# Performance work log

Hardware: AMD Instinct MI355X
Metric: run time of the kernel (lower is better)

## Reference

```python
import jax, jax.numpy as jnp
import numpy as np

N_NODES = 100000
N_EDGES = 1600000
IN_CH = 128
HID = 128
OUT_CH = 40


def setup_inputs() -> dict:
    key = jax.random.key(0)
    ks = jax.random.split(key, 8)
    x = jax.random.normal(ks[0], (N_NODES, IN_CH), dtype=jnp.float32)
    edge_index = jax.random.randint(ks[1], (2, N_EDGES), 0, N_NODES, dtype=jnp.int64)
    s1 = 1.0 / np.sqrt(IN_CH)
    s2 = 1.0 / np.sqrt(HID)
    # SAGEConv layer 1: lin_l (applied to aggregated neighbors, has bias), lin_r (applied to root, no bias)
    Wl1 = jax.random.uniform(ks[2], (IN_CH, HID), jnp.float32, -s1, s1)
    b1 = jnp.zeros((HID,), jnp.float32)
    Wr1 = jax.random.uniform(ks[3], (IN_CH, HID), jnp.float32, -s1, s1)
    # SAGEConv layer 2
    Wl2 = jax.random.uniform(ks[4], (HID, OUT_CH), jnp.float32, -s2, s2)
    b2 = jnp.zeros((OUT_CH,), jnp.float32)
    Wr2 = jax.random.uniform(ks[5], (HID, OUT_CH), jnp.float32, -s2, s2)
    return {"x": x, "edge_index": edge_index, "Wl1": Wl1, "b1": b1, "Wr1": Wr1,
            "Wl2": Wl2, "b2": b2, "Wr2": Wr2}


def _sage_conv(x, src, dst, Wl, b, Wr):
    # mean-aggregate source-node features onto target nodes (PyG SAGEConv, aggr='mean')
    msg_sum = jax.ops.segment_sum(x[src], dst, num_segments=N_NODES)  # [N, F]
    deg = jax.ops.segment_sum(jnp.ones((src.shape[0],), x.dtype), dst, num_segments=N_NODES)
    aggr = msg_sum / jnp.maximum(deg, 1.0)[:, None]
    return aggr @ Wl + b + x @ Wr


def reference(x, edge_index, Wl1, b1, Wr1, Wl2, b2, Wr2):
    src, dst = edge_index[0], edge_index[1]
    h = _sage_conv(x, src, dst, Wl1, b1, Wr1)
    h = jax.nn.relu(h)  # dropout is identity in eval mode
    h = _sage_conv(h, src, dst, Wl2, b2, Wr2)
    return jax.nn.log_softmax(h, axis=-1)
```

## Files before the change

### kernel.cpp

```cpp
#include <hip/hip_runtime.h>
#include <math.h>

#define NN 100000
#define NE 1600000
#define NBUK ((NN + 255) / 256)
#define CAP 5120
#define NBLK_A 500
#define EPB (NE / NBLK_A)
#define GPB (EPB / 4)
#define MT ((NN + 127) / 128)
#define MPAD ((size_t)MT * 128)
#define PACK_B 192
#define CVT_B0 (NBLK_A + PACK_B)
#define FRONT_GRID 2048

typedef __attribute__((ext_vector_type(8))) short short8;
typedef __attribute__((ext_vector_type(4))) float f32x4;
typedef __attribute__((ext_vector_type(4))) int i32x4;
typedef unsigned short ushort_t;
typedef unsigned int uint_t;

__device__ inline ushort_t f2bf(float f) {
    uint_t u = __builtin_bit_cast(uint_t, f);
    u += 0x7FFFu + ((u >> 16) & 1u);
    return (ushort_t)(u >> 16);
}
__device__ inline float bits2f(uint_t u) { return __builtin_bit_cast(float, u); }
__device__ inline float lo16(uint_t u) { return bits2f(u << 16); }
__device__ inline float hi16(uint_t u) { return bits2f(u & 0xFFFF0000u); }

__device__ inline void gload_lds16(const void* g, void* l) {
    __builtin_amdgcn_global_load_lds(
        (const __attribute__((address_space(1))) unsigned int*)g,
        (__attribute__((address_space(3))) unsigned int*)l, 16, 0, 0);
}

__global__ __launch_bounds__(256) void front(const float* __restrict__ x,
                                             ushort_t* __restrict__ xb,
                                             const float* __restrict__ Wl1,
                                             const float* __restrict__ Wr1,
                                             const float* __restrict__ Wl2,
                                             const float* __restrict__ Wr2,
                                             ushort_t* __restrict__ W1T,
                                             ushort_t* __restrict__ W2T,
                                             const int* __restrict__ ei,
                                             int* __restrict__ bhist) {
    __shared__ int h[NBUK];
    int bid = blockIdx.x, tid = threadIdx.x;
    if (bid < NBLK_A) {
        for (int i = tid; i < NBUK; i += 256) h[i] = 0;
        __syncthreads();
        const i32x4* dsts = (const i32x4*)(ei + NE + bid * EPB);
        for (int g = tid; g < GPB; g += 256) {
            i32x4 d = __builtin_nontemporal_load(dsts + g);
#pragma unroll
            for (int j = 0; j < 4; ++j) atomicAdd(&h[d[j] >> 8], 1);
        }
        __syncthreads();
        for (int i = tid; i < NBUK; i += 256)
            if (h[i]) atomicAdd(&bhist[i], h[i]);
    } else if (bid < CVT_B0) {
        int gid = (bid - NBLK_A) * 256 + tid;
        if (gid < 256 * 128) {
            int n = gid >> 7, k = gid & 127;
            float v = (n < 128) ? Wl1[k * 128 + n] : Wr1[k * 128 + (n - 128)];
            W1T[gid] = f2bf(v);
        } else {
            int g = gid - 256 * 128;
            if (g < 128 * 128) {
                int n = g >> 7, k = g & 127;
                float v = 0.0f;
                if (n < 40)      v = Wl2[k * 40 + n];
                else if (n < 80) v = Wr2[k * 40 + (n - 40)];
                W2T[g] = f2bf(v);
            }
        }
    } else {
        const int total = NN * 128 / 8;
        const int nb = FRONT_GRID - CVT_B0;
        const f32x4* src = (const f32x4*)x;
        for (int g = (bid - CVT_B0) * 256 + tid; g < total; g += nb * 256) {
            f32x4 v0 = __builtin_nontemporal_load(src + (size_t)g * 2);
            f32x4 v1 = __builtin_nontemporal_load(src + (size_t)g * 2 + 1);
            i32x4 o;
            o[0] = ((uint_t)f2bf(v0[1]) << 16) | (uint_t)f2bf(v0[0]);
            o[1] = ((uint_t)f2bf(v0[3]) << 16) | (uint_t)f2bf(v0[2]);
            o[2] = ((uint_t)f2bf(v1[1]) << 16) | (uint_t)f2bf(v1[0]);
            o[3] = ((uint_t)f2bf(v1[3]) << 16) | (uint_t)f2bf(v1[2]);
            *(i32x4*)(xb + (size_t)g * 8) = o;
        }
    }
}

__global__ __launch_bounds__(512) void scan_buckets(const int* __restrict__ bhist,
                                                    int* __restrict__ boff,
                                                    int* __restrict__ gcur,
                                                    int* __restrict__ offsets) {
    __shared__ int part[512];
    int t = threadIdx.x;
    int v = (t < NBUK) ? bhist[t] : 0;
    part[t] = v;
    __syncthreads();
    for (int d = 1; d < 512; d <<= 1) {
        int tmp = (t >= d) ? part[t - d] : 0;
        __syncthreads();
        part[t] += tmp;
        __syncthreads();
    }
    if (t <= NBUK) {
        int excl = (t == 0) ? 0 : part[t - 1];
        boff[t] = excl;
        if (t < NBUK) gcur[t] = excl;
    }
    if (t == 0) offsets[NN] = NE;
}

__global__ __launch_bounds__(256) void bin_pass(const int* __restrict__ ei,
                                                int* __restrict__ gcur,
                                                int* __restrict__ pairs) {
    __shared__ int h[NBUK];
    __shared__ int base[NBUK];
    int tid = threadIdx.x;
    for (int i = tid; i < NBUK; i += 256) h[i] = 0;
    __syncthreads();
    int e0 = blockIdx.x * EPB;
    const i32x4* dsts = (const i32x4*)(ei + NE + e0);
    const i32x4* srcs = (const i32x4*)(ei + e0);
    for (int g = tid; g < GPB; g += 256) {
        i32x4 d = __builtin_nontemporal_load(dsts + g);
#pragma unroll
        for (int j = 0; j < 4; ++j) atomicAdd(&h[d[j] >> 8], 1);
    }
    __syncthreads();
    for (int i = tid; i < NBUK; i += 256) {
        int c = h[i];
        base[i] = c ? atomicAdd(&gcur[i], c) : 0;
        h[i] = 0;
    }
    __syncthreads();
    for (int g = tid; g < GPB; g += 256) {
        i32x4 d = __builtin_nontemporal_load(dsts + g);
        i32x4 s = __builtin_nontemporal_load(srcs + g);
#pragma unroll
        for (int j = 0; j < 4; ++j) {
            int buk = d[j] >> 8;
            int pos = base[buk] + atomicAdd(&h[buk], 1);
            pairs[pos] = (s[j] << 8) | (d[j] & 255);
        }
    }
}

__global__ __launch_bounds__(256) void sort_buckets(const int* __restrict__ boff,
                                                    const int* __restrict__ pairs,
                                                    int* __restrict__ offsets,
                                                    int* __restrict__ ssrc) {
    __shared__ int plds[CAP];
    __shared__ int slds[CAP];
    __shared__ int cnt[256];
    __shared__ int excl[256];
    int buk = blockIdx.x, tid = threadIdx.x;
    int bstart = boff[buk], bend = boff[buk + 1];
    int count = min(bend - bstart, CAP);
    int lo = buk << 8;
    cnt[tid] = 0;
    __syncthreads();
    for (int j = tid; j < count; j += 256) {
        int p = pairs[bstart + j];
        plds[j] = p;
        atomicAdd(&cnt[p & 255], 1);
    }
    __syncthreads();
    int c = cnt[tid];
    excl[tid] = c;
    __syncthreads();
    for (int d = 1; d < 256; d <<= 1) {
        int tmp = (tid >= d) ? excl[tid - d] : 0;
        __syncthreads();
        excl[tid] += tmp;
        __syncthreads();
    }
    int myExcl = excl[tid] - c;
    __syncthreads();
    excl[tid] = myExcl;
    cnt[tid] = 0;
    __syncthreads();
    for (int j = tid; j < count; j += 256) {
        int p = plds[j];
        int loc = p & 255;
        int pos = excl[loc] + atomicAdd(&cnt[loc], 1);
        slds[pos] = p >> 8;
    }
    __syncthreads();
    for (int j = tid; j < count; j += 256) ssrc[bstart + j] = slds[j];
    if (lo + tid < NN) offsets[lo + tid] = bstart + myExcl;
}

__global__ __launch_bounds__(256, 2) void gemm_mfma(const ushort_t* __restrict__ A,
                                                    const ushort_t* __restrict__ Bt,
                                                    ushort_t* __restrict__ G,
                                                    ushort_t* __restrict__ Croot,
                                                    int M, int split, int rootEnd, int gstride) {
    __shared__ __align__(16) char As[128 * 256];
    __shared__ __align__(16) char Bs[128 * 256];
    int tid = threadIdx.x;
    int lane = tid & 63, wid = tid >> 6;
    int quad = lane >> 4, l15 = lane & 15;
    int wm = (wid & 1) * 64, wn = (wid >> 1) * 64;
    int mBase = blockIdx.x * 128, nBase = blockIdx.y * 128;
    int rootW = rootEnd - split;

    const char* aT = (const char*)(A + (size_t)mBase * 128);
    const char* bT = (const char*)(Bt + (size_t)nBase * 128);
#pragma unroll
    for (int ii = 0; ii < 8; ++ii) {
        int rr = (wid * 8 + ii) * 4 + quad;
        int src = rr * 256 + ((l15 * 16) ^ ((rr & 7) << 4));
        int ldsb = (wid * 8 + ii) * 1024;
        gload_lds16(aT + src, As + ldsb);
        gload_lds16(bT + src, Bs + ldsb);
    }
    asm volatile("s_waitcnt vmcnt(0)" ::: "memory");
    __syncthreads();

    f32x4 acc[4][4];
#pragma unroll
    for (int i = 0; i < 4; ++i)
#pragma unroll
        for (int j = 0; j < 4; ++j) acc[i][j] = (f32x4){0.f, 0.f, 0.f, 0.f};

#pragma unroll
    for (int kk = 0; kk < 4; ++kk) {
        int kByte = kk * 64 + quad * 16;
        short8 af[4], bfr[4];
#pragma unroll
        for (int i = 0; i < 4; ++i) {
            int row = wm + i * 16 + l15;
            af[i] = *(const short8*)(As + row * 256 + (kByte ^ ((row & 7) << 4)));
        }
#pragma unroll
        for (int j = 0; j < 4; ++j) {
            int row = wn + j * 16 + l15;
            bfr[j] = *(const short8*)(Bs + row * 256 + (kByte ^ ((row & 7) << 4)));
        }
#pragma unroll
        for (int i = 0; i < 4; ++i)
#pragma unroll
            for (int j = 0; j < 4; ++j)
                acc[i][j] = __builtin_amdgcn_mfma_f32_16x16x32_bf16(af[i], bfr[j],
                                                                    acc[i][j], 0, 0, 0);
    }

#pragma unroll
    for (int i = 0; i < 4; ++i) {
#pragma unroll
        for (int r = 0; r < 4; ++r) {
            int m = mBase + wm + i * 16 + quad * 4 + r;
            if (m >= M) continue;
#pragma unroll
            for (int j = 0; j < 4; ++j) {
                int n = nBase + wn + j * 16 + l15;
                float v = acc[i][j][r];
                if (n < split) G[(size_t)m * gstride + n] = f2bf(v);
                else if (n < rootEnd) Croot[(size_t)m * rootW + (n - split)] = f2bf(v);
            }
        }
    }
}

__global__ __launch_bounds__(256) void aggregate1(const int* __restrict__ offsets,
                                                  const int* __restrict__ ssrc,
                                                  const ushort_t* __restrict__ G1,
                                                  const ushort_t* __restrict__ C1root,
                                                  const float* __restrict__ b1,
                                                  ushort_t* __restrict__ s1b) {
    int w = (blockIdx.x * blockDim.x + threadIdx.x) >> 6;
    int lane = threadIdx.x & 63;
    if (w >= NN) return;
    int start = offsets[w], end = offsets[w + 1];
    int g = lane >> 4, q = lane & 15;
    const char* Gb = (const char*)G1;
    int qb = q << 4;
    float a0 = 0.f, a1 = 0.f, a2 = 0.f, a3 = 0.f, a4 = 0.f, a5 = 0.f, a6 = 0.f, a7 = 0.f;
    for (int base = start; base < end; base += 64) {
        int cnt = min(64, end - base);
        int idx = (base + lane < end) ? ssrc[base + lane] : 0;
        int j = 0;
        for (; j + 16 <= cnt; j += 16) {
            int s0 = __shfl(idx, j + g, 64);
            int s1 = __shfl(idx, j + 4 + g, 64);
            int s2 = __shfl(idx, j + 8 + g, 64);
            int s3 = __shfl(idx, j + 12 + g, 64);
            uint4 u0 = *(const uint4*)(Gb + (s0 << 8) + qb);
            uint4 u1 = *(const uint4*)(Gb + (s1 << 8) + qb);
            uint4 u2 = *(const uint4*)(Gb + (s2 << 8) + qb);
            uint4 u3 = *(const uint4*)(Gb + (s3 << 8) + qb);
            a0 += (lo16(u0.x) + lo16(u1.x)) + (lo16(u2.x) + lo16(u3.x));
            a1 += (hi16(u0.x) + hi16(u1.x)) + (hi16(u2.x) + hi16(u3.x));
            a2 += (lo16(u0.y) + lo16(u1.y)) + (lo16(u2.y) + lo16(u3.y));
            a3 += (hi16(u0.y) + hi16(u1.y)) + (hi16(u2.y) + hi16(u3.y));
            a4 += (lo16(u0.z) + lo16(u1.z)) + (lo16(u2.z) + lo16(u3.z));
            a5 += (hi16(u0.z) + hi16(u1.z)) + (hi16(u2.z) + hi16(u3.z));
            a6 += (lo16(u0.w) + lo16(u1.w)) + (lo16(u2.w) + lo16(u3.w));
            a7 += (hi16(u0.w) + hi16(u1.w)) + (hi16(u2.w) + hi16(u3.w));
        }
        for (; j + 8 <= cnt; j += 8) {
            int s0 = __shfl(idx, j + g, 64);
            int s1 = __shfl(idx, j + 4 + g, 64);
            uint4 u0 = *(const uint4*)(Gb + (s0 << 8) + qb);
            uint4 u1 = *(const uint4*)(Gb + (s1 << 8) + qb);
            a0 += lo16(u0.x) + lo16(u1.x);
            a1 += hi16(u0.x) + hi16(u1.x);
            a2 += lo16(u0.y) + lo16(u1.y);
            a3 += hi16(u0.y) + hi16(u1.y);
            a4 += lo16(u0.z) + lo16(u1.z);
            a5 += hi16(u0.z) + hi16(u1.z);
            a6 += lo16(u0.w) + lo16(u1.w);
            a7 += hi16(u0.w) + hi16(u1.w);
        }
        for (; j < cnt; j += 4) {
            int e = j + g;
            int s0 = __shfl(idx, (e < cnt) ? e : 0, 64);
            if (e < cnt) {
                uint4 u0 = *(const uint4*)(Gb + (s0 << 8) + qb);
                a0 += lo16(u0.x); a1 += hi16(u0.x);
                a2 += lo16(u0.y); a3 += hi16(u0.y);
                a4 += lo16(u0.z); a5 += hi16(u0.z);
                a6 += lo16(u0.w); a7 += hi16(u0.w);
            }
        }
    }
    a0 += __shfl_xor(a0, 16, 64); a0 += __shfl_xor(a0, 32, 64);
    a1 += __shfl_xor(a1, 16, 64); a1 += __shfl_xor(a1, 32, 64);
    a2 += __shfl_xor(a2, 16, 64); a2 += __shfl_xor(a2, 32, 64);
    a3 += __shfl_xor(a3, 16, 64); a3 += __shfl_xor(a3, 32, 64);
    a4 += __shfl_xor(a4, 16, 64); a4 += __shfl_xor(a4, 32, 64);
    a5 += __shfl_xor(a5, 16, 64); a5 += __shfl_xor(a5, 32, 64);
    a6 += __shfl_xor(a6, 16, 64); a6 += __shfl_xor(a6, 32, 64);
    a7 += __shfl_xor(a7, 16, 64); a7 += __shfl_xor(a7, 32, 64);
    if (g == 0) {
        float inv = 1.0f / fmaxf((float)(end - start), 1.0f);
        uint4 rv = *(const uint4*)((const char*)C1root + (size_t)w * 256 + qb);
        float4 c0 = *(const float4*)(b1 + q * 8);
        float4 c1 = *(const float4*)(b1 + q * 8 + 4);
        float h0 = fmaxf(a0 * inv + c0.x + lo16(rv.x), 0.f);
        float h1 = fmaxf(a1 * inv + c0.y + hi16(rv.x), 0.f);
        float h2 = fmaxf(a2 * inv + c0.z + lo16(rv.y), 0.f);
        float h3 = fmaxf(a3 * inv + c0.w + hi16(rv.y), 0.f);
        float h4 = fmaxf(a4 * inv + c1.x + lo16(rv.z), 0.f);
        float h5 = fmaxf(a5 * inv + c1.y + hi16(rv.z), 0.f);
        float h6 = fmaxf(a6 * inv + c1.z + lo16(rv.w), 0.f);
        float h7 = fmaxf(a7 * inv + c1.w + hi16(rv.w), 0.f);
        uint4 o;
        o.x = ((uint_t)f2bf(h1) << 16) | (uint_t)f2bf(h0);
        o.y = ((uint_t)f2bf(h3) << 16) | (uint_t)f2bf(h2);
        o.z = ((uint_t)f2bf(h5) << 16) | (uint_t)f2bf(h4);
        o.w = ((uint_t)f2bf(h7) << 16) | (uint_t)f2bf(h6);
        *(uint4*)((char*)s1b + (size_t)w * 256 + qb) = o;
    }
}

__global__ __launch_bounds__(256) void aggregate2(const int* __restrict__ offsets,
                                                  const int* __restrict__ ssrc,
                                                  const ushort_t* __restrict__ G2,
                                                  const ushort_t* __restrict__ C2root,
                                                  const float* __restrict__ b2,
                                                  float* __restrict__ out) {
    int w = (blockIdx.x * blockDim.x + threadIdx.x) >> 6;
    int lane = threadIdx.x & 63;
    if (w >= NN) return;
    int start = offsets[w], end = offsets[w + 1];
    int g = lane >> 4, q = lane & 15;
    bool act = q < 10;
    int qb = q << 3;
    const char* Gb = (const char*)G2;
    float a0 = 0.f, a1 = 0.f, a2 = 0.f, a3 = 0.f;
    for (int base = start; base < end; base += 64) {
        int cnt = min(64, end - base);
        int idx = (base + lane < end) ? ssrc[base + lane] : 0;
        int j = 0;
        for (; j + 16 <= cnt; j += 16) {
            int s0 = __shfl(idx, j + g, 64);
            int s1 = __shfl(idx, j + 4 + g, 64);
            int s2 = __shfl(idx, j + 8 + g, 64);
            int s3 = __shfl(idx, j + 12 + g, 64);
            if (act) {
                uint2 u0 = *(const uint2*)(Gb + (size_t)s0 * 80 + qb);
                uint2 u1 = *(const uint2*)(Gb + (size_t)s1 * 80 + qb);
                uint2 u2 = *(const uint2*)(Gb + (size_t)s2 * 80 + qb);
                uint2 u3 = *(const uint2*)(Gb + (size_t)s3 * 80 + qb);
                a0 += (lo16(u0.x) + lo16(u1.x)) + (lo16(u2.x) + lo16(u3.x));
                a1 += (hi16(u0.x) + hi16(u1.x)) + (hi16(u2.x) + hi16(u3.x));
                a2 += (lo16(u0.y) + lo16(u1.y)) + (lo16(u2.y) + lo16(u3.y));
                a3 += (hi16(u0.y) + hi16(u1.y)) + (hi16(u2.y) + hi16(u3.y));
            }
        }
        for (; j + 8 <= cnt; j += 8) {
            int s0 = __shfl(idx, j + g, 64);
            int s1 = __shfl(idx, j + 4 + g, 64);
            if (act) {
                uint2 u0 = *(const uint2*)(Gb + (size_t)s0 * 80 + qb);
                uint2 u1 = *(const uint2*)(Gb + (size_t)s1 * 80 + qb);
                a0 += lo16(u0.x) + lo16(u1.x);
                a1 += hi16(u0.x) + hi16(u1.x);
                a2 += lo16(u0.y) + lo16(u1.y);
                a3 += hi16(u0.y) + hi16(u1.y);
            }
        }
        for (; j < cnt; j += 4) {
            int e = j + g;
            int s0 = __shfl(idx, (e < cnt) ? e : 0, 64);
            if (act && e < cnt) {
                uint2 u0 = *(const uint2*)(Gb + (size_t)s0 * 80 + qb);
                a0 += lo16(u0.x); a1 += hi16(u0.x);
                a2 += lo16(u0.y); a3 += hi16(u0.y);
            }
        }
    }
    a0 += __shfl_xor(a0, 16, 64); a0 += __shfl_xor(a0, 32, 64);
    a1 += __shfl_xor(a1, 16, 64); a1 += __shfl_xor(a1, 32, 64);
    a2 += __shfl_xor(a2, 16, 64); a2 += __shfl_xor(a2, 32, 64);
    a3 += __shfl_xor(a3, 16, 64); a3 += __shfl_xor(a3, 32, 64);
    if (g == 0) {
        float inv = 1.0f / fmaxf((float)(end - start), 1.0f);
        float v0 = -INFINITY, v1 = -INFINITY, v2 = -INFINITY, v3 = -INFINITY;
        if (act) {
            uint2 rv = *(const uint2*)((const char*)C2root + (size_t)w * 80 + qb);
            float4 bb = *(const float4*)(b2 + q * 4);
            v0 = a0 * inv + bb.x + lo16(rv.x);
            v1 = a1 * inv + bb.y + hi16(rv.x);
            v2 = a2 * inv + bb.z + lo16(rv.y);
            v3 = a3 * inv + bb.w + hi16(rv.y);
        }
        float m = fmaxf(fmaxf(v0, v1), fmaxf(v2, v3));
#pragma unroll
        for (int d = 8; d >= 1; d >>= 1) m = fmaxf(m, __shfl_xor(m, d, 64));
        float e = act ? (expf(v0 - m) + expf(v1 - m)) + (expf(v2 - m) + expf(v3 - m)) : 0.f;
#pragma unroll
        for (int d = 8; d >= 1; d >>= 1) e += __shfl_xor(e, d, 64);
        float lse = m + logf(e);
        if (act) {
            float4 o = make_float4(v0 - lse, v1 - lse, v2 - lse, v3 - lse);
            *(float4*)(out + (size_t)w * 40 + q * 4) = o;
        }
    }
}

extern "C" void kernel_launch(void* const* d_in, const int* in_sizes, int n_in,
                              void* d_out, int out_size, void* d_ws, size_t ws_size,
                              hipStream_t stream) {
    const float* x   = (const float*)d_in[0];
    const int*   ei  = (const int*)d_in[1];
    const float* Wl1 = (const float*)d_in[2];
    const float* b1  = (const float*)d_in[3];
    const float* Wr1 = (const float*)d_in[4];
    const float* Wl2 = (const float*)d_in[5];
    const float* b2  = (const float*)d_in[6];
    const float* Wr2 = (const float*)d_in[7];
    float* out = (float*)d_out;

    char* ws = (char*)d_ws;
    size_t off = 0;
    auto alloc = [&](size_t bytes) -> void* {
        void* p = ws + off;
        off = (off + bytes + 255) & ~(size_t)255;
        return p;
    };
    int*      bhist   = (int*)alloc((size_t)NBUK * 4);
    int*      boff    = (int*)alloc((size_t)(NBUK + 1) * 4);
    int*      gcur    = (int*)alloc((size_t)NBUK * 4);
    int*      pairs   = (int*)alloc((size_t)NE * 4);
    int*      offsets = (int*)alloc((size_t)(NN + 1) * 4);
    int*      ssrc    = (int*)alloc((size_t)NE * 4);
    ushort_t* W1T     = (ushort_t*)alloc((size_t)256 * 128 * 2);
    ushort_t* W2T     = (ushort_t*)alloc((size_t)128 * 128 * 2);
    ushort_t* xb      = (ushort_t*)alloc(MPAD * 128 * 2);
    ushort_t* G1      = (ushort_t*)alloc((size_t)NN * 128 * 2);
    ushort_t* C1root  = (ushort_t*)alloc((size_t)NN * 128 * 2);
    ushort_t* s1b     = (ushort_t*)alloc(MPAD * 128 * 2);
    ushort_t* G2      = (ushort_t*)alloc((size_t)NN * 40 * 2);
    ushort_t* C2root  = (ushort_t*)alloc((size_t)NN * 40 * 2);

    hipMemsetAsync(bhist, 0, (size_t)NBUK * 4, stream);

    front<<<FRONT_GRID, 256, 0, stream>>>(x, xb, Wl1, Wr1, Wl2, Wr2, W1T, W2T, ei, bhist);
    scan_buckets<<<1, 512, 0, stream>>>(bhist, boff, gcur, offsets);
    bin_pass<<<NBLK_A, 256, 0, stream>>>(ei, gcur, pairs);
    sort_buckets<<<NBUK, 256, 0, stream>>>(boff, pairs, offsets, ssrc);

    dim3 g1(MT, 2);
    gemm_mfma<<<g1, 256, 0, stream>>>(xb, W1T, G1, C1root, NN, 128, 256, 128);

    aggregate1<<<(NN * 64 + 255) / 256, 256, 0, stream>>>(offsets, ssrc, G1, C1root, b1, s1b);

    dim3 g2(MT, 1);
    gemm_mfma<<<g2, 256, 0, stream>>>(s1b, W2T, G2, C2root, NN, 40, 80, 40);

    aggregate2<<<(NN * 64 + 255) / 256, 256, 0, stream>>>(offsets, ssrc, G2, C2root, b2, out);
}
```

Baseline: 331.2 us.

## Fuse layer-1 aggregation with layer-2 GEMM and reuse per-block bucket histograms

Each wave now aggregates 16 destination rows of layer 1, stages the bf16 hidden rows in a swizzled LDS tile, and immediately runs the 16x80 layer-2 MFMA GEMM from LDS. This removes the s1b round trip through global memory and one kernel launch. The front kernel also stores its per-block bucket histograms so bin_pass can skip re-reading dst and recounting. G2 is padded to a 128-byte row stride so aggregate2 can use shift addressing. In exchange, each wave handles 16 rows serially, which cuts parallelism in the gather phase, and the W2T operand is reloaded from global memory by every wave.

```diff
diff --git a/kernel.cpp b/kernel.cpp
--- a/kernel.cpp
+++ b/kernel.cpp
@@ -10,6 +10,7 @@
 #define GPB (EPB / 4)
 #define MT ((NN + 127) / 128)
 #define MPAD ((size_t)MT * 128)
+#define NT2 (NN / 16)
 #define PACK_B 192
 #define CVT_B0 (NBLK_A + PACK_B)
 #define FRONT_GRID 2048
@@ -44,7 +45,8 @@
                                              ushort_t* __restrict__ W1T,
                                              ushort_t* __restrict__ W2T,
                                              const int* __restrict__ ei,
-                                             int* __restrict__ bhist) {
+                                             int* __restrict__ bhist,
+                                             int* __restrict__ bhp) {
     __shared__ int h[NBUK];
     int bid = blockIdx.x, tid = threadIdx.x;
     if (bid < NBLK_A) {
@@ -57,8 +59,11 @@
             for (int j = 0; j < 4; ++j) atomicAdd(&h[d[j] >> 8], 1);
         }
         __syncthreads();
-        for (int i = tid; i < NBUK; i += 256)
-            if (h[i]) atomicAdd(&bhist[i], h[i]);
+        for (int i = tid; i < NBUK; i += 256) {
+            int c = h[i];
+            bhp[bid * NBUK + i] = c;
+            if (c) atomicAdd(&bhist[i], c);
+        }
     } else if (bid < CVT_B0) {
         int gid = (bid - NBLK_A) * 256 + tid;
         if (gid < 256 * 128) {
@@ -116,28 +121,22 @@
 }
 
 __global__ __launch_bounds__(256) void bin_pass(const int* __restrict__ ei,
+                                                const int* __restrict__ bhp,
                                                 int* __restrict__ gcur,
                                                 int* __restrict__ pairs) {
     __shared__ int h[NBUK];
     __shared__ int base[NBUK];
-    int tid = threadIdx.x;
-    for (int i = tid; i < NBUK; i += 256) h[i] = 0;
-    __syncthreads();
-    int e0 = blockIdx.x * EPB;
+    int bid = blockIdx.x, tid = threadIdx.x;
+    const int* myh = bhp + bid * NBUK;
+    for (int i = tid; i < NBUK; i += 256) {
+        int c = myh[i];
+        base[i] = c ? atomicAdd(&gcur[i], c) : 0;
+        h[i] = 0;
+    }
+    __syncthreads();
+    int e0 = bid * EPB;
     const i32x4* dsts = (const i32x4*)(ei + NE + e0);
     const i32x4* srcs = (const i32x4*)(ei + e0);
-    for (int g = tid; g < GPB; g += 256) {
-        i32x4 d = __builtin_nontemporal_load(dsts + g);
-#pragma unroll
-        for (int j = 0; j < 4; ++j) atomicAdd(&h[d[j] >> 8], 1);
-    }
-    __syncthreads();
-    for (int i = tid; i < NBUK; i += 256) {
-        int c = h[i];
-        base[i] = c ? atomicAdd(&gcur[i], c) : 0;
-        h[i] = 0;
-    }
-    __syncthreads();
     for (int g = tid; g < GPB; g += 256) {
         i32x4 d = __builtin_nontemporal_load(dsts + g);
         i32x4 s = __builtin_nontemporal_load(srcs + g);
@@ -267,95 +266,134 @@
     }
 }
 
-__global__ __launch_bounds__(256) void aggregate1(const int* __restrict__ offsets,
+__global__ __launch_bounds__(256) void agg1_gemm2(const int* __restrict__ offsets,
                                                   const int* __restrict__ ssrc,
                                                   const ushort_t* __restrict__ G1,
                                                   const ushort_t* __restrict__ C1root,
                                                   const float* __restrict__ b1,
-                                                  ushort_t* __restrict__ s1b) {
-    int w = (blockIdx.x * blockDim.x + threadIdx.x) >> 6;
-    int lane = threadIdx.x & 63;
-    if (w >= NN) return;
-    int start = offsets[w], end = offsets[w + 1];
+                                                  const ushort_t* __restrict__ W2T,
+                                                  ushort_t* __restrict__ G2,
+                                                  ushort_t* __restrict__ C2root) {
+    __shared__ __align__(16) char stage[4][16 * 256];
+    int tid = threadIdx.x, lane = tid & 63, wid = tid >> 6;
     int g = lane >> 4, q = lane & 15;
+    int qb = q << 4;
+    int t = blockIdx.x * 4 + wid;
+    int m0 = t * 16;
+    char* sw = stage[wid];
     const char* Gb = (const char*)G1;
-    int qb = q << 4;
-    float a0 = 0.f, a1 = 0.f, a2 = 0.f, a3 = 0.f, a4 = 0.f, a5 = 0.f, a6 = 0.f, a7 = 0.f;
-    for (int base = start; base < end; base += 64) {
-        int cnt = min(64, end - base);
-        int idx = (base + lane < end) ? ssrc[base + lane] : 0;
-        int j = 0;
-        for (; j + 16 <= cnt; j += 16) {
-            int s0 = __shfl(idx, j + g, 64);
-            int s1 = __shfl(idx, j + 4 + g, 64);
-            int s2 = __shfl(idx, j + 8 + g, 64);
-            int s3 = __shfl(idx, j + 12 + g, 64);
-            uint4 u0 = *(const uint4*)(Gb + (s0 << 8) + qb);
-            uint4 u1 = *(const uint4*)(Gb + (s1 << 8) + qb);
-            uint4 u2 = *(const uint4*)(Gb + (s2 << 8) + qb);
-            uint4 u3 = *(const uint4*)(Gb + (s3 << 8) + qb);
-            a0 += (lo16(u0.x) + lo16(u1.x)) + (lo16(u2.x) + lo16(u3.x));
-            a1 += (hi16(u0.x) + hi16(u1.x)) + (hi16(u2.x) + hi16(u3.x));
-            a2 += (lo16(u0.y) + lo16(u1.y)) + (lo16(u2.y) + lo16(u3.y));
-            a3 += (hi16(u0.y) + hi16(u1.y)) + (hi16(u2.y) + hi16(u3.y));
-            a4 += (lo16(u0.z) + lo16(u1.z)) + (lo16(u2.z) + lo16(u3.z));
-            a5 += (hi16(u0.z) + hi16(u1.z)) + (hi16(u2.z) + hi16(u3.z));
-            a6 += (lo16(u0.w) + lo16(u1.w)) + (lo16(u2.w) + lo16(u3.w));
-            a7 += (hi16(u0.w) + hi16(u1.w)) + (hi16(u2.w) + hi16(u3.w));
-        }
-        for (; j + 8 <= cnt; j += 8) {
-            int s0 = __shfl(idx, j + g, 64);
-            int s1 = __shfl(idx, j + 4 + g, 64);
-            uint4 u0 = *(const uint4*)(Gb + (s0 << 8) + qb);
-            uint4 u1 = *(const uint4*)(Gb + (s1 << 8) + qb);
-            a0 += lo16(u0.x) + lo16(u1.x);
-            a1 += hi16(u0.x) + hi16(u1.x);
-            a2 += lo16(u0.y) + lo16(u1.y);
-            a3 += hi16(u0.y) + hi16(u1.y);
-            a4 += lo16(u0.z) + lo16(u1.z);
-            a5 += hi16(u0.z) + hi16(u1.z);
-            a6 += lo16(u0.w) + lo16(u1.w);
-            a7 += hi16(u0.w) + hi16(u1.w);
-        }
-        for (; j < cnt; j += 4) {
-            int e = j + g;
-            int s0 = __shfl(idx, (e < cnt) ? e : 0, 64);
-            if (e < cnt) {
-                uint4 u0 = *(const uint4*)(Gb + (s0 << 8) + qb);
-                a0 += lo16(u0.x); a1 += hi16(u0.x);
-                a2 += lo16(u0.y); a3 += hi16(u0.y);
-                a4 += lo16(u0.z); a5 += hi16(u0.z);
-                a6 += lo16(u0.w); a7 += hi16(u0.w);
-            }
-        }
-    }
-    a0 += __shfl_xor(a0, 16, 64); a0 += __shfl_xor(a0, 32, 64);
-    a1 += __shfl_xor(a1, 16, 64); a1 += __shfl_xor(a1, 32, 64);
-    a2 += __shfl_xor(a2, 16, 64); a2 += __shfl_xor(a2, 32, 64);
-    a3 += __shfl_xor(a3, 16, 64); a3 += __shfl_xor(a3, 32, 64);
-    a4 += __shfl_xor(a4, 16, 64); a4 += __shfl_xor(a4, 32, 64);
-    a5 += __shfl_xor(a5, 16, 64); a5 += __shfl_xor(a5, 32, 64);
-    a6 += __shfl_xor(a6, 16, 64); a6 += __shfl_xor(a6, 32, 64);
-    a7 += __shfl_xor(a7, 16, 64); a7 += __shfl_xor(a7, 32, 64);
-    if (g == 0) {
-        float inv = 1.0f / fmaxf((float)(end - start), 1.0f);
-        uint4 rv = *(const uint4*)((const char*)C1root + (size_t)w * 256 + qb);
-        float4 c0 = *(const float4*)(b1 + q * 8);
-        float4 c1 = *(const float4*)(b1 + q * 8 + 4);
-        float h0 = fmaxf(a0 * inv + c0.x + lo16(rv.x), 0.f);
-        float h1 = fmaxf(a1 * inv + c0.y + hi16(rv.x), 0.f);
-        float h2 = fmaxf(a2 * inv + c0.z + lo16(rv.y), 0.f);
-        float h3 = fmaxf(a3 * inv + c0.w + hi16(rv.y), 0.f);
-        float h4 = fmaxf(a4 * inv + c1.x + lo16(rv.z), 0.f);
-        float h5 = fmaxf(a5 * inv + c1.y + hi16(rv.z), 0.f);
-        float h6 = fmaxf(a6 * inv + c1.z + lo16(rv.w), 0.f);
-        float h7 = fmaxf(a7 * inv + c1.w + hi16(rv.w), 0.f);
-        uint4 o;
-        o.x = ((uint_t)f2bf(h1) << 16) | (uint_t)f2bf(h0);
-        o.y = ((uint_t)f2bf(h3) << 16) | (uint_t)f2bf(h2);
-        o.z = ((uint_t)f2bf(h5) << 16) | (uint_t)f2bf(h4);
-        o.w = ((uint_t)f2bf(h7) << 16) | (uint_t)f2bf(h6);
-        *(uint4*)((char*)s1b + (size_t)w * 256 + qb) = o;
+
+    for (int pass = 0; pass < 16; ++pass) {
+        int w = m0 + pass;
+        if (w < NN) {
+            int start = offsets[w], end = offsets[w + 1];
+            float a0 = 0.f, a1 = 0.f, a2 = 0.f, a3 = 0.f,
+                  a4 = 0.f, a5 = 0.f, a6 = 0.f, a7 = 0.f;
+            for (int base = start; base < end; base += 64) {
+                int cnt = min(64, end - base);
+                int idx = (base + lane < end) ? ssrc[base + lane] : 0;
+                int j = 0;
+                for (; j + 16 <= cnt; j += 16) {
+                    int s0 = __shfl(idx, j + g, 64);
+                    int s1 = __shfl(idx, j + 4 + g, 64);
+                    int s2 = __shfl(idx, j + 8 + g, 64);
+                    int s3 = __shfl(idx, j + 12 + g, 64);
+                    uint4 u0 = *(const uint4*)(Gb + (s0 << 8) + qb);
+                    uint4 u1 = *(const uint4*)(Gb + (s1 << 8) + qb);
+                    uint4 u2 = *(const uint4*)(Gb + (s2 << 8) + qb);
+                    uint4 u3 = *(const uint4*)(Gb + (s3 << 8) + qb);
+                    a0 += (lo16(u0.x) + lo16(u1.x)) + (lo16(u2.x) + lo16(u3.x));
+                    a1 += (hi16(u0.x) + hi16(u1.x)) + (hi16(u2.x) + hi16(u3.x));
+                    a2 += (lo16(u0.y) + lo16(u1.y)) + (lo16(u2.y) + lo16(u3.y));
+                    a3 += (hi16(u0.y) + hi16(u1.y)) + (hi16(u2.y) + hi16(u3.y));
+                    a4 += (lo16(u0.z) + lo16(u1.z)) + (lo16(u2.z) + lo16(u3.z));
+                    a5 += (hi16(u0.z) + hi16(u1.z)) + (hi16(u2.z) + hi16(u3.z));
+                    a6 += (lo16(u0.w) + lo16(u1.w)) + (lo16(u2.w) + lo16(u3.w));
+                    a7 += (hi16(u0.w) + hi16(u1.w)) + (hi16(u2.w) + hi16(u3.w));
+                }
+                for (; j + 8 <= cnt; j += 8) {
+                    int s0 = __shfl(idx, j + g, 64);
+                    int s1 = __shfl(idx, j + 4 + g, 64);
+                    uint4 u0 = *(const uint4*)(Gb + (s0 << 8) + qb);
+                    uint4 u1 = *(const uint4*)(Gb + (s1 << 8) + qb);
+                    a0 += lo16(u0.x) + lo16(u1.x);
+                    a1 += hi16(u0.x) + hi16(u1.x);
+                    a2 += lo16(u0.y) + lo16(u1.y);
+                    a3 += hi16(u0.y) + hi16(u1.y);
+                    a4 += lo16(u0.z) + lo16(u1.z);
+                    a5 += hi16(u0.z) + hi16(u1.z);
+                    a6 += lo16(u0.w) + lo16(u1.w);
+                    a7 += hi16(u0.w) + hi16(u1.w);
+                }
+                for (; j < cnt; j += 4) {
+                    int e = j + g;
+                    int s0 = __shfl(idx, (e < cnt) ? e : 0, 64);
+                    if (e < cnt) {
+                        uint4 u0 = *(const uint4*)(Gb + (s0 << 8) + qb);
+                        a0 += lo16(u0.x); a1 += hi16(u0.x);
+                        a2 += lo16(u0.y); a3 += hi16(u0.y);
+                        a4 += lo16(u0.z); a5 += hi16(u0.z);
+                        a6 += lo16(u0.w); a7 += hi16(u0.w);
+                    }
+                }
+            }
+            a0 += __shfl_xor(a0, 16, 64); a0 += __shfl_xor(a0, 32, 64);
+            a1 += __shfl_xor(a1, 16, 64); a1 += __shfl_xor(a1, 32, 64);
+            a2 += __shfl_xor(a2, 16, 64); a2 += __shfl_xor(a2, 32, 64);
+            a3 += __shfl_xor(a3, 16, 64); a3 += __shfl_xor(a3, 32, 64);
+            a4 += __shfl_xor(a4, 16, 64); a4 += __shfl_xor(a4, 32, 64);
+            a5 += __shfl_xor(a5, 16, 64); a5 += __shfl_xor(a5, 32, 64);
+            a6 += __shfl_xor(a6, 16, 64); a6 += __shfl_xor(a6, 32, 64);
+            a7 += __shfl_xor(a7, 16, 64); a7 += __shfl_xor(a7, 32, 64);
+            if (g == 0) {
+                float inv = 1.0f / fmaxf((float)(end - start), 1.0f);
+                uint4 rv = *(const uint4*)((const char*)C1root + (size_t)w * 256 + qb);
+                float4 c0 = *(const float4*)(b1 + q * 8);
+                float4 c1 = *(const float4*)(b1 + q * 8 + 4);
+                float h0 = fmaxf(a0 * inv + c0.x + lo16(rv.x), 0.f);
+                float h1 = fmaxf(a1 * inv + c0.y + hi16(rv.x), 0.f);
+                float h2 = fmaxf(a2 * inv + c0.z + lo16(rv.y), 0.f);
+                float h3 = fmaxf(a3 * inv + c0.w + hi16(rv.y), 0.f);
+                float h4 = fmaxf(a4 * inv + c1.x + lo16(rv.z), 0.f);
+                float h5 = fmaxf(a5 * inv + c1.y + hi16(rv.z), 0.f);
+                float h6 = fmaxf(a6 * inv + c1.z + lo16(rv.w), 0.f);
+                float h7 = fmaxf(a7 * inv + c1.w + hi16(rv.w), 0.f);
+                uint4 o;
+                o.x = ((uint_t)f2bf(h1) << 16) | (uint_t)f2bf(h0);
+                o.y = ((uint_t)f2bf(h3) << 16) | (uint_t)f2bf(h2);
+                o.z = ((uint_t)f2bf(h5) << 16) | (uint_t)f2bf(h4);
+                o.w = ((uint_t)f2bf(h7) << 16) | (uint_t)f2bf(h6);
+                *(uint4*)(sw + pass * 256 + ((q ^ (pass & 7)) << 4)) = o;
+            }
+        }
+    }
+    __syncthreads();
+    if (m0 >= NN) return;
+
+    int quad = g, l15 = q;
+    f32x4 acc[5];
+#pragma unroll
+    for (int j = 0; j < 5; ++j) acc[j] = (f32x4){0.f, 0.f, 0.f, 0.f};
+#pragma unroll
+    for (int kk = 0; kk < 4; ++kk) {
+        int cu = kk * 4 + quad;
+        short8 af = *(const short8*)(sw + l15 * 256 + ((cu ^ (l15 & 7)) << 4));
+#pragma unroll
+        for (int j = 0; j < 5; ++j) {
+            short8 bfr = *(const short8*)(W2T + (size_t)(j * 16 + l15) * 128 + kk * 32 + quad * 8);
+            acc[j] = __builtin_amdgcn_mfma_f32_16x16x32_bf16(af, bfr, acc[j], 0, 0, 0);
+        }
+    }
+#pragma unroll
+    for (int j = 0; j < 5; ++j) {
+#pragma unroll
+        for (int r = 0; r < 4; ++r) {
+            int m = m0 + quad * 4 + r;
+            int n = j * 16 + l15;
+            float v = acc[j][r];
+            if (n < 40) G2[(size_t)m * 64 + n] = f2bf(v);
+            else if (n < 80) C2root[(size_t)m * 40 + (n - 40)] = f2bf(v);
+        }
     }
 }
 
@@ -384,10 +422,10 @@
             int s2 = __shfl(idx, j + 8 + g, 64);
             int s3 = __shfl(idx, j + 12 + g, 64);
             if (act) {
-                uint2 u0 = *(const uint2*)(Gb + (size_t)s0 * 80 + qb);
-                uint2 u1 = *(const uint2*)(Gb + (size_t)s1 * 80 + qb);
-                uint2 u2 = *(const uint2*)(Gb + (size_t)s2 * 80 + qb);
-                uint2 u3 = *(const uint2*)(Gb + (size_t)s3 * 80 + qb);
+                uint2 u0 = *(const uint2*)(Gb + (s0 << 7) + qb);
+                uint2 u1 = *(const uint2*)(Gb + (s1 << 7) + qb);
+                uint2 u2 = *(const uint2*)(Gb + (s2 << 7) + qb);
+                uint2 u3 = *(const uint2*)(Gb + (s3 << 7) + qb);
                 a0 += (lo16(u0.x) + lo16(u1.x)) + (lo16(u2.x) + lo16(u3.x));
                 a1 += (hi16(u0.x) + hi16(u1.x)) + (hi16(u2.x) + hi16(u3.x));
                 a2 += (lo16(u0.y) + lo16(u1.y)) + (lo16(u2.y) + lo16(u3.y));
@@ -398,8 +436,8 @@
             int s0 = __shfl(idx, j + g, 64);
             int s1 = __shfl(idx, j + 4 + g, 64);
             if (act) {
-                uint2 u0 = *(const uint2*)(Gb + (size_t)s0 * 80 + qb);
-                uint2 u1 = *(const uint2*)(Gb + (size_t)s1 * 80 + qb);
+                uint2 u0 = *(const uint2*)(Gb + (s0 << 7) + qb);
+                uint2 u1 = *(const uint2*)(Gb + (s1 << 7) + qb);
                 a0 += lo16(u0.x) + lo16(u1.x);
                 a1 += hi16(u0.x) + hi16(u1.x);
                 a2 += lo16(u0.y) + lo16(u1.y);
@@ -410,7 +448,7 @@
             int e = j + g;
             int s0 = __shfl(idx, (e < cnt) ? e : 0, 64);
             if (act && e < cnt) {
-                uint2 u0 = *(const uint2*)(Gb + (size_t)s0 * 80 + qb);
+                uint2 u0 = *(const uint2*)(Gb + (s0 << 7) + qb);
                 a0 += lo16(u0.x); a1 += hi16(u0.x);
                 a2 += lo16(u0.y); a3 += hi16(u0.y);
             }
@@ -468,6 +506,7 @@
     int*      bhist   = (int*)alloc((size_t)NBUK * 4);
     int*      boff    = (int*)alloc((size_t)(NBUK + 1) * 4);
     int*      gcur    = (int*)alloc((size_t)NBUK * 4);
+    int*      bhp     = (int*)alloc((size_t)NBLK_A * NBUK * 4);
     int*      pairs   = (int*)alloc((size_t)NE * 4);
     int*      offsets = (int*)alloc((size_t)(NN + 1) * 4);
     int*      ssrc    = (int*)alloc((size_t)NE * 4);
@@ -476,24 +515,20 @@
     ushort_t* xb      = (ushort_t*)alloc(MPAD * 128 * 2);
     ushort_t* G1      = (ushort_t*)alloc((size_t)NN * 128 * 2);
     ushort_t* C1root  = (ushort_t*)alloc((size_t)NN * 128 * 2);
-    ushort_t* s1b     = (ushort_t*)alloc(MPAD * 128 * 2);
-    ushort_t* G2      = (ushort_t*)alloc((size_t)NN * 40 * 2);
+    ushort_t* G2      = (ushort_t*)alloc((size_t)NN * 64 * 2);
     ushort_t* C2root  = (ushort_t*)alloc((size_t)NN * 40 * 2);
 
     hipMemsetAsync(bhist, 0, (size_t)NBUK * 4, stream);
 
-    front<<<FRONT_GRID, 256, 0, stream>>>(x, xb, Wl1, Wr1, Wl2, Wr2, W1T, W2T, ei, bhist);
+    front<<<FRONT_GRID, 256, 0, stream>>>(x, xb, Wl1, Wr1, Wl2, Wr2, W1T, W2T, ei, bhist, bhp);
     scan_buckets<<<1, 512, 0, stream>>>(bhist, boff, gcur, offsets);
-    bin_pass<<<NBLK_A, 256, 0, stream>>>(ei, gcur, pairs);
+    bin_pass<<<NBLK_A, 256, 0, stream>>>(ei, bhp, gcur, pairs);
     sort_buckets<<<NBUK, 256, 0, stream>>>(boff, pairs, offsets, ssrc);
 
     dim3 g1(MT, 2);
     gemm_mfma<<<g1, 256, 0, stream>>>(xb, W1T, G1, C1root, NN, 128, 256, 128);
 
-    aggregate1<<<(NN * 64 + 255) / 256, 256, 0, stream>>>(offsets, ssrc, G1, C1root, b1, s1b);
-
-    dim3 g2(MT, 1);
-    gemm_mfma<<<g2, 256, 0, stream>>>(s1b, W2T, G2, C2root, NN, 40, 80, 40);
+    agg1_gemm2<<<(NT2 + 3) / 4, 256, 0, stream>>>(offsets, ssrc, G1, C1root, b1, W2T, G2, C2root);
 
     aggregate2<<<(NN * 64 + 255) / 256, 256, 0, stream>>>(offsets, ssrc, G2, C2root, b2, out);
 }
```

New measurement: 352.7 us. 1.06x slower.
